# Kernel tuning notes

Hardware: AMD Instinct MI355X
Metric: run time of the kernel (lower is better)

## Reference

```python
import jax, jax.numpy as jnp
import numpy as np

M_MARGIN = 0.25
GAMMA = 64.0
EPS = 1e-5


def _circle_loss_one_way(enc, dec):
    # enc, dec: [N, D]. Faithful to the torch rotate-concat construction:
    # cos_sim[j, k] = cosine(enc[j], dec[(j + k) % N]); column 0 is the positive.
    N = enc.shape[0]
    dot = enc @ dec.T                                   # [N, N]
    en = jnp.sqrt(jnp.sum(enc * enc, axis=1, keepdims=True))   # [N, 1]
    dn = jnp.sqrt(jnp.sum(dec * dec, axis=1, keepdims=True))   # [N, 1]
    S = dot / (en * dn.T + EPS)                         # [N, N] cosine sims
    r = jnp.arange(N)
    idx = (r[:, None] + r[None, :]) % N                 # [N, N] rolled column index
    cos_sim = jnp.take_along_axis(S, idx, axis=1)       # [N, N]
    sp = cos_sim[:, 0:1]                                # [N, 1] positives (diag of S)
    sn = cos_sim[:, 1:]                                 # [N, N-1] negatives
    ap = jnp.maximum(-jax.lax.stop_gradient(sp) + 1.0 + M_MARGIN, 0.0)
    an = jnp.maximum(jax.lax.stop_gradient(sn) + M_MARGIN, 0.0)
    delta_p = 1.0 - M_MARGIN
    delta_n = M_MARGIN
    logit_p = -ap * (sp - delta_p) * GAMMA              # [N, 1]
    logit_n = an * (sn - delta_n) * GAMMA               # [N, N-1]
    lse_n = jax.nn.logsumexp(logit_n, axis=0)           # [N-1]
    lse_p = jax.nn.logsumexp(logit_p, axis=0)           # [1] (cols of repeated sp are identical)
    return jax.nn.softplus(lse_n + lse_p)               # [N-1]


def reference(encoder_output, decoder_output):
    loss_a = _circle_loss_one_way(encoder_output, decoder_output)
    loss_b = _circle_loss_one_way(decoder_output, encoder_output)
    return jnp.mean((loss_a + loss_b) / 2.0)


def setup_inputs() -> dict:
    key = jax.random.key(0)
    k1, k2 = jax.random.split(key)
    N, D = 8192, 128
    return {
        "encoder_output": jax.random.normal(k1, (N, D), dtype=jnp.float32),
        "decoder_output": jax.random.normal(k2, (N, D), dtype=jnp.float32),
    }
```

## Files before the change

kernel.cpp:

```cpp
#include <hip/hip_runtime.h>
#include <hip/hip_bf16.h>

#define NN 8192

using f32x4 = __attribute__((ext_vector_type(4))) float;

#if __has_builtin(__builtin_amdgcn_exp2f)
#define EXP2(x) __builtin_amdgcn_exp2f(x)
#else
#define EXP2(x) __expf((x) * 0.69314718056f)
#endif

__device__ __forceinline__ void gl_lds16(const void* g, void* l) {
  __builtin_amdgcn_global_load_lds(
      (const __attribute__((address_space(1))) unsigned int*)(unsigned long long)g,
      (__attribute__((address_space(3))) unsigned int*)(unsigned int)(unsigned long long)l,
      16, 0, 0);
}

#if __has_builtin(__builtin_amdgcn_cvt_pk_fp8_f32)
__device__ __forceinline__ unsigned pk4_fp8(float x0, float x1, float x2, float x3) {
  unsigned w = (unsigned)__builtin_amdgcn_cvt_pk_fp8_f32(x0, x1, 0, false);
  w = (unsigned)__builtin_amdgcn_cvt_pk_fp8_f32(x2, x3, (int)w, true);
  return w;
}
#else
__device__ __forceinline__ unsigned f8_1(float f) {
  unsigned u = __float_as_uint(f);
  unsigned s = (u >> 24) & 0x80u;
  float a = fabsf(f);
  if (a < 0.015625f) {
    unsigned m = (unsigned)rintf(a * 512.0f);
    return s | (m > 7u ? 8u : m);
  }
  if (a > 448.0f) return s | 0x7Eu;
  unsigned au = u & 0x7FFFFFFFu;
  unsigned e = (au >> 23) - 127u + 7u;
  unsigned m23 = au & 0x7FFFFFu;
  unsigned m = m23 >> 20;
  unsigned rem = m23 & 0xFFFFFu;
  if (rem > 0x80000u || (rem == 0x80000u && (m & 1u))) {
    if (++m == 8u) { m = 0u; ++e; }
  }
  return s | (e << 3) | m;
}
__device__ __forceinline__ unsigned pk4_fp8(float x0, float x1, float x2, float x3) {
  return f8_1(x0) | (f8_1(x1) << 8) | (f8_1(x2) << 16) | (f8_1(x3) << 24);
}
#endif

__global__ __launch_bounds__(256) void k_prep(const float* __restrict__ enc,
                                              const float* __restrict__ dec,
                                              uint2* __restrict__ A8,
                                              uint2* __restrict__ B8,
                                              float* __restrict__ logit_p,
                                              float* __restrict__ bandsum,
                                              unsigned* __restrict__ counter) {
  const int t = threadIdx.x;
  const int l16 = t & 15;
  const int row = blockIdx.x * 16 + (t >> 4);
  const int tid = blockIdx.x * 256 + t;
  if (tid < 64 * 256) bandsum[tid] = 0.0f;
  if (tid == 64 * 256) *counter = 0u;

  const float4* e4 = reinterpret_cast<const float4*>(enc) + (size_t)row * 32 + l16 * 2;
  const float4* d4 = reinterpret_cast<const float4*>(dec) + (size_t)row * 32 + l16 * 2;
  float4 e0 = e4[0], e1 = e4[1];
  float4 d0 = d4[0], d1 = d4[1];

  float se = e0.x*e0.x + e0.y*e0.y + e0.z*e0.z + e0.w*e0.w
           + e1.x*e1.x + e1.y*e1.y + e1.z*e1.z + e1.w*e1.w;
  float sd = d0.x*d0.x + d0.y*d0.y + d0.z*d0.z + d0.w*d0.w
           + d1.x*d1.x + d1.y*d1.y + d1.z*d1.z + d1.w*d1.w;
  float sp = e0.x*d0.x + e0.y*d0.y + e0.z*d0.z + e0.w*d0.w
           + e1.x*d1.x + e1.y*d1.y + e1.z*d1.z + e1.w*d1.w;
#pragma unroll
  for (int off = 1; off < 16; off <<= 1) {
    se += __shfl_xor(se, off);
    sd += __shfl_xor(sd, off);
    sp += __shfl_xor(sp, off);
  }
  float ie = rsqrtf(se), id = rsqrtf(sd);

  uint2 ua, ub;
  ua.x = pk4_fp8(e0.x * ie, e0.y * ie, e0.z * ie, e0.w * ie);
  ua.y = pk4_fp8(e1.x * ie, e1.y * ie, e1.z * ie, e1.w * ie);
  ub.x = pk4_fp8(d0.x * id, d0.y * id, d0.z * id, d0.w * id);
  ub.y = pk4_fp8(d1.x * id, d1.y * id, d1.z * id, d1.w * id);
  A8[(size_t)row * 16 + l16] = ua;
  B8[(size_t)row * 16 + l16] = ub;

  if (l16 == 0) {
    float en = se * ie, dn = sd * id;
    float s  = sp / (en * dn + 1e-5f);
    logit_p[row] = -fmaxf(1.25f - s, 0.0f) * (s - 0.75f) * 64.0f;
  }
}

__global__ __launch_bounds__(256, 2) void k_main(const unsigned char* __restrict__ A,
                                                 const unsigned char* __restrict__ B,
                                                 float* __restrict__ bandsum,
                                                 const float* __restrict__ logit_p,
                                                 unsigned* __restrict__ counter,
                                                 float* __restrict__ out) {
  __shared__ __align__(16) unsigned char As[2 * 16384];
  __shared__ __align__(16) unsigned char Bs[2 * 16384];
  __shared__ float part[4][256];
  __shared__ unsigned lastFlag;

  const int t  = threadIdx.x;
  const int T  = blockIdx.x;
  const int sp = blockIdx.y;

#pragma unroll
  for (int q = 0; q < 4; ++q) part[q][t] = 0.0f;

  const int lane = t & 63;
  const int w = t >> 6, wrow = w >> 1, wcol = w & 1;
  const int l15 = lane & 15, quad = lane >> 4;
  const int x7 = l15 & 7;
  const int qh = quad >> 1, ql8 = (quad & 1) * 8;

  const int rl = t >> 3;
  const int lgoff = rl * 128 + ((t & 7) ^ (rl & 7)) * 16;
  const int lloff = t * 16;

  const char* Ab = (const char*)A;
  const char* Bb = (const char*)B;

  float dreg[28];
#pragma unroll
  for (int i = 0; i < 28; ++i) dreg[i] = 0.0f;

  const int arow = (wrow * 64 + l15) * 128;
  const int brow = (wcol * 64 + l15) * 128;

  {
    const int by = sp * 8;
    const int bx = (by + T) & 63;
    const char* Ag = Ab + (size_t)by * 16384 + lgoff;
    const char* Bg = Bb + (size_t)bx * 16384 + lgoff;
#pragma unroll
    for (int j = 0; j < 4; ++j) {
      gl_lds16(Ag + j * 4096, (char*)As + j * 4096 + lloff);
      gl_lds16(Bg + j * 4096, (char*)Bs + j * 4096 + lloff);
    }
  }
  __syncthreads();

  for (int it = 0; it < 8; ++it) {
    const int p = it & 1;

    if (it < 7) {
      const int by = sp * 8 + it + 1;
      const int bx = (by + T) & 63;
      const char* Ag = Ab + (size_t)by * 16384 + lgoff;
      const char* Bg = Bb + (size_t)bx * 16384 + lgoff;
      char* Ad = (char*)As + (p ^ 1) * 16384 + lloff;
      char* Bd = (char*)Bs + (p ^ 1) * 16384 + lloff;
#pragma unroll
      for (int j = 0; j < 4; ++j) {
        gl_lds16(Ag + j * 4096, Ad + j * 4096);
        gl_lds16(Bg + j * 4096, Bd + j * 4096);
      }
    }

    f32x4 acc[4][4];
    const f32x4 zv = {0.f, 0.f, 0.f, 0.f};
#pragma unroll
    for (int r = 0; r < 4; ++r)
#pragma unroll
      for (int c = 0; c < 4; ++c) acc[r][c] = zv;

    const char* Abuf = (const char*)As + p * 16384;
    const char* Bbuf = (const char*)Bs + p * 16384;

#pragma unroll
    for (int ks = 0; ks < 4; ++ks) {
      long a[4], b[4];
      const int off = (((ks * 2 + qh) ^ x7) * 16) + ql8;
#pragma unroll
      for (int r = 0; r < 4; ++r)
        a[r] = *reinterpret_cast<const long*>(Abuf + arow + r * 2048 + off);
#pragma unroll
      for (int c = 0; c < 4; ++c)
        b[c] = *reinterpret_cast<const long*>(Bbuf + brow + c * 2048 + off);
#pragma unroll
      for (int r = 0; r < 4; ++r)
#pragma unroll
        for (int c = 0; c < 4; ++c)
          acc[r][c] = __builtin_amdgcn_mfma_f32_16x16x32_fp8_fp8(a[r], b[c], acc[r][c], 0, 0, 0);
    }

#pragma unroll
    for (int dlt = -3; dlt <= 3; ++dlt) {
#pragma unroll
      for (int g = 0; g < 4; ++g) {
        float s = 0.0f;
#pragma unroll
        for (int r = 0; r < 4; ++r) {
          int c = r + dlt;
          if (c < 0 || c > 3) continue;
          float sn = acc[r][c][g];
          float an = fmaxf(sn + 0.25f, 0.0f);
          float u  = fmaf(sn, 92.332483f, -23.083121f);
          s += EXP2(an * u);
        }
        dreg[(dlt + 3) * 4 + g] += s;
      }
    }

    __syncthreads();
  }

  const int  Qoff = (wcol - wrow) * 64 + 127;
  const int  v    = l15 - quad * 4;
  const bool leader = (quad == 0) || (l15 <= 3);
  const bool ok1 = (l15 <= 11) && (quad <= 2);
  const bool ok2 = (l15 <= 7)  && (quad <= 1);

#pragma unroll
  for (int dlt = -3; dlt <= 3; ++dlt) {
#pragma unroll
    for (int g = 0; g < 4; ++g) {
      float s = dreg[(dlt + 3) * 4 + g];
      float t1 = __shfl_down(s, 20); s += ok1 ? t1 : 0.0f;
      float t2 = __shfl_down(s, 40); s += ok2 ? t2 : 0.0f;
      int ld = Qoff + dlt * 16 - g + v;
      if (leader) unsafeAtomicAdd(&part[w][ld], s);
    }
  }
  __syncthreads();

  if (t < 255) {
    float vv = part[0][t] + part[1][t] + part[2][t] + part[3][t];
    unsafeAtomicAdd(&bandsum[T * 256 + t], vv);
  }

  __syncthreads();
  if (t == 0) lastFlag = (atomicAdd(counter, 1u) == 511u) ? 1u : 0u;
  __syncthreads();
  if (!lastFlag) return;

  __threadfence();
  float* sm = part[0];

  float lp[32];
#pragma unroll
  for (int k = 0; k < 32; ++k) lp[k] = logit_p[t + 256 * k];

  float m = lp[0];
#pragma unroll
  for (int k = 1; k < 32; ++k) m = fmaxf(m, lp[k]);
#pragma unroll
  for (int off = 32; off; off >>= 1) m = fmaxf(m, __shfl_down(m, off));
  if (lane == 0) sm[w] = m;
  __syncthreads();
  m = fmaxf(fmaxf(sm[0], sm[1]), fmaxf(sm[2], sm[3]));
  __syncthreads();

  float s = 0.0f;
#pragma unroll
  for (int k = 0; k < 32; ++k) s += __expf(lp[k] - m);
#pragma unroll
  for (int off = 32; off; off >>= 1) s += __shfl_down(s, off);
  if (lane == 0) sm[w] = s;
  __syncthreads();
  s = sm[0] + sm[1] + sm[2] + sm[3];
  float lse_p = m + __logf(s);
  __syncthreads();

  const int o  = t & 127;
  const int hi = t >> 7;
  float bs1[32], bs2[32];
#pragma unroll
  for (int k = 0; k < 32; ++k) {
    int Ta = hi + 2 * k;
    bs1[k] = bandsum[Ta * 256 + o + 127];
    bs2[k] = o ? bandsum[((Ta + 1) & 63) * 256 + o - 1] : 0.0f;
  }
  float acc = 0.0f;
#pragma unroll
  for (int k = 0; k < 32; ++k) {
    if (t == 0 && k == 0) continue;
    float se = bs1[k] + bs2[k];
    float x = __logf(se) + lse_p;
    acc += fmaxf(x, 0.0f) + __logf(1.0f + __expf(-fabsf(x)));
  }
#pragma unroll
  for (int off = 32; off; off >>= 1) acc += __shfl_down(acc, off);
  if (lane == 0) sm[w] = acc;
  __syncthreads();
  if (t == 0) out[0] = (sm[0] + sm[1] + sm[2] + sm[3]) * (1.0f / 8191.0f);
}

extern "C" void kernel_launch(void* const* d_in, const int* in_sizes, int n_in,
                              void* d_out, int out_size, void* d_ws, size_t ws_size,
                              hipStream_t stream) {
  const float* enc = (const float*)d_in[0];
  const float* dec = (const float*)d_in[1];
  float* ws = (float*)d_ws;

  float*    logit_p = ws;
  float*    bandsum = ws + 8192;
  unsigned* counter = (unsigned*)(ws + 8192 + 16384);
  uint2*    A8      = (uint2*)(ws + 8192 + 16384 + 256);
  uint2*    B8      = (uint2*)((char*)A8 + 1048576);
  float*    out     = (float*)d_out;

  k_prep<<<NN / 16, 256, 0, stream>>>(enc, dec, A8, B8, logit_p, bandsum, counter);
  dim3 grid(64, 8);
  k_main<<<grid, 256, 0, stream>>>((const unsigned char*)A8, (const unsigned char*)B8,
                                   bandsum, logit_p, counter, out);
}
```

Baseline: 96.51 us.

## Split K into halves to shrink LDS tiles and double grid/occupancy

Each 128x128 fp8 tile is now loaded as two 64-byte K halves, which halves the LDS staging buffers. The accumulator persists across the pair, and the epilogue runs only after the second half. The grid doubles to 64x16 blocks with four tiles each, and launch bounds move to 4 blocks per SM so more waves can hide latency. The trade-off is twice as many synchronizations per tile and tighter register limits that may cause spills.

```diff
diff --git a/kernel.cpp b/kernel.cpp
--- a/kernel.cpp
+++ b/kernel.cpp
@@ -97,14 +97,14 @@
   }
 }
 
-__global__ __launch_bounds__(256, 2) void k_main(const unsigned char* __restrict__ A,
+__global__ __launch_bounds__(256, 4) void k_main(const unsigned char* __restrict__ A,
                                                  const unsigned char* __restrict__ B,
                                                  float* __restrict__ bandsum,
                                                  const float* __restrict__ logit_p,
                                                  unsigned* __restrict__ counter,
                                                  float* __restrict__ out) {
-  __shared__ __align__(16) unsigned char As[2 * 16384];
-  __shared__ __align__(16) unsigned char Bs[2 * 16384];
+  __shared__ __align__(16) unsigned char As[2 * 8192];
+  __shared__ __align__(16) unsigned char Bs[2 * 8192];
   __shared__ float part[4][256];
   __shared__ unsigned lastFlag;
 
@@ -118,11 +118,10 @@
   const int lane = t & 63;
   const int w = t >> 6, wrow = w >> 1, wcol = w & 1;
   const int l15 = lane & 15, quad = lane >> 4;
-  const int x7 = l15 & 7;
+  const int x3 = l15 & 3;
   const int qh = quad >> 1, ql8 = (quad & 1) * 8;
 
-  const int rl = t >> 3;
-  const int lgoff = rl * 128 + ((t & 7) ^ (rl & 7)) * 16;
+  const int lg    = (t >> 2) * 128 + (((t & 3) ^ ((t >> 2) & 3)) * 16);
   const int lloff = t * 16;
 
   const char* Ab = (const char*)A;
@@ -132,59 +131,64 @@
 #pragma unroll
   for (int i = 0; i < 28; ++i) dreg[i] = 0.0f;
 
-  const int arow = (wrow * 64 + l15) * 128;
-  const int brow = (wcol * 64 + l15) * 128;
+  const int arow = (wrow * 64 + l15) * 64;
+  const int brow = (wcol * 64 + l15) * 64;
 
   {
-    const int by = sp * 8;
+    const int by = sp * 4;
     const int bx = (by + T) & 63;
-    const char* Ag = Ab + (size_t)by * 16384 + lgoff;
-    const char* Bg = Bb + (size_t)bx * 16384 + lgoff;
-#pragma unroll
-    for (int j = 0; j < 4; ++j) {
-      gl_lds16(Ag + j * 4096, (char*)As + j * 4096 + lloff);
-      gl_lds16(Bg + j * 4096, (char*)Bs + j * 4096 + lloff);
-    }
-  }
-  __syncthreads();
-
-  for (int it = 0; it < 8; ++it) {
-    const int p = it & 1;
-
-    if (it < 7) {
-      const int by = sp * 8 + it + 1;
+    const char* Ag = Ab + (size_t)by * 16384 + lg;
+    const char* Bg = Bb + (size_t)bx * 16384 + lg;
+#pragma unroll
+    for (int j = 0; j < 2; ++j) {
+      gl_lds16(Ag + j * 8192, (char*)As + j * 4096 + lloff);
+      gl_lds16(Bg + j * 8192, (char*)Bs + j * 4096 + lloff);
+    }
+  }
+  __syncthreads();
+
+  f32x4 acc[4][4];
+
+#pragma unroll
+  for (int h = 0; h < 8; ++h) {
+    const int p = h & 1;
+
+    if (h < 7) {
+      const int hn = h + 1;
+      const int by = sp * 4 + (hn >> 1);
       const int bx = (by + T) & 63;
-      const char* Ag = Ab + (size_t)by * 16384 + lgoff;
-      const char* Bg = Bb + (size_t)bx * 16384 + lgoff;
-      char* Ad = (char*)As + (p ^ 1) * 16384 + lloff;
-      char* Bd = (char*)Bs + (p ^ 1) * 16384 + lloff;
-#pragma unroll
-      for (int j = 0; j < 4; ++j) {
-        gl_lds16(Ag + j * 4096, Ad + j * 4096);
-        gl_lds16(Bg + j * 4096, Bd + j * 4096);
+      const char* Ag = Ab + (size_t)by * 16384 + (hn & 1) * 64 + lg;
+      const char* Bg = Bb + (size_t)bx * 16384 + (hn & 1) * 64 + lg;
+      char* Ad = (char*)As + (p ^ 1) * 8192 + lloff;
+      char* Bd = (char*)Bs + (p ^ 1) * 8192 + lloff;
+#pragma unroll
+      for (int j = 0; j < 2; ++j) {
+        gl_lds16(Ag + j * 8192, Ad + j * 4096);
+        gl_lds16(Bg + j * 8192, Bd + j * 4096);
       }
     }
 
-    f32x4 acc[4][4];
-    const f32x4 zv = {0.f, 0.f, 0.f, 0.f};
-#pragma unroll
-    for (int r = 0; r < 4; ++r)
-#pragma unroll
-      for (int c = 0; c < 4; ++c) acc[r][c] = zv;
-
-    const char* Abuf = (const char*)As + p * 16384;
-    const char* Bbuf = (const char*)Bs + p * 16384;
-
-#pragma unroll
-    for (int ks = 0; ks < 4; ++ks) {
+    if (p == 0) {
+      const f32x4 zv = {0.f, 0.f, 0.f, 0.f};
+#pragma unroll
+      for (int r = 0; r < 4; ++r)
+#pragma unroll
+        for (int c = 0; c < 4; ++c) acc[r][c] = zv;
+    }
+
+    const char* Abuf = (const char*)As + p * 8192;
+    const char* Bbuf = (const char*)Bs + p * 8192;
+
+#pragma unroll
+    for (int ks = 0; ks < 2; ++ks) {
       long a[4], b[4];
-      const int off = (((ks * 2 + qh) ^ x7) * 16) + ql8;
+      const int off = (((ks * 2 + qh) ^ x3) * 16) + ql8;
 #pragma unroll
       for (int r = 0; r < 4; ++r)
-        a[r] = *reinterpret_cast<const long*>(Abuf + arow + r * 2048 + off);
+        a[r] = *reinterpret_cast<const long*>(Abuf + arow + r * 1024 + off);
 #pragma unroll
       for (int c = 0; c < 4; ++c)
-        b[c] = *reinterpret_cast<const long*>(Bbuf + brow + c * 2048 + off);
+        b[c] = *reinterpret_cast<const long*>(Bbuf + brow + c * 1024 + off);
 #pragma unroll
       for (int r = 0; r < 4; ++r)
 #pragma unroll
@@ -192,21 +196,23 @@
           acc[r][c] = __builtin_amdgcn_mfma_f32_16x16x32_fp8_fp8(a[r], b[c], acc[r][c], 0, 0, 0);
     }
 
-#pragma unroll
-    for (int dlt = -3; dlt <= 3; ++dlt) {
-#pragma unroll
-      for (int g = 0; g < 4; ++g) {
-        float s = 0.0f;
-#pragma unroll
-        for (int r = 0; r < 4; ++r) {
-          int c = r + dlt;
-          if (c < 0 || c > 3) continue;
-          float sn = acc[r][c][g];
-          float an = fmaxf(sn + 0.25f, 0.0f);
-          float u  = fmaf(sn, 92.332483f, -23.083121f);
-          s += EXP2(an * u);
+    if (p == 1) {
+#pragma unroll
+      for (int dlt = -3; dlt <= 3; ++dlt) {
+#pragma unroll
+        for (int g = 0; g < 4; ++g) {
+          float s = 0.0f;
+#pragma unroll
+          for (int r = 0; r < 4; ++r) {
+            int c = r + dlt;
+            if (c < 0 || c > 3) continue;
+            float sn = acc[r][c][g];
+            float an = fmaxf(sn + 0.25f, 0.0f);
+            float u  = fmaf(sn, 92.332483f, -23.083121f);
+            s += EXP2(an * u);
+          }
+          dreg[(dlt + 3) * 4 + g] += s;
         }
-        dreg[(dlt + 3) * 4 + g] += s;
       }
     }
 
@@ -238,7 +244,7 @@
   }
 
   __syncthreads();
-  if (t == 0) lastFlag = (atomicAdd(counter, 1u) == 511u) ? 1u : 0u;
+  if (t == 0) lastFlag = (atomicAdd(counter, 1u) == 1023u) ? 1u : 0u;
   __syncthreads();
   if (!lastFlag) return;
 
@@ -279,17 +285,17 @@
     bs1[k] = bandsum[Ta * 256 + o + 127];
     bs2[k] = o ? bandsum[((Ta + 1) & 63) * 256 + o - 1] : 0.0f;
   }
-  float acc = 0.0f;
+  float tacc = 0.0f;
 #pragma unroll
   for (int k = 0; k < 32; ++k) {
     if (t == 0 && k == 0) continue;
     float se = bs1[k] + bs2[k];
     float x = __logf(se) + lse_p;
-    acc += fmaxf(x, 0.0f) + __logf(1.0f + __expf(-fabsf(x)));
-  }
-#pragma unroll
-  for (int off = 32; off; off >>= 1) acc += __shfl_down(acc, off);
-  if (lane == 0) sm[w] = acc;
+    tacc += fmaxf(x, 0.0f) + __logf(1.0f + __expf(-fabsf(x)));
+  }
+#pragma unroll
+  for (int off = 32; off; off >>= 1) tacc += __shfl_down(tacc, off);
+  if (lane == 0) sm[w] = tacc;
   __syncthreads();
   if (t == 0) out[0] = (sm[0] + sm[1] + sm[2] + sm[3]) * (1.0f / 8191.0f);
 }
@@ -309,7 +315,7 @@
   float*    out     = (float*)d_out;
 
   k_prep<<<NN / 16, 256, 0, stream>>>(enc, dec, A8, B8, logit_p, bandsum, counter);
-  dim3 grid(64, 8);
+  dim3 grid(64, 16);
   k_main<<<grid, 256, 0, stream>>>((const unsigned char*)A8, (const unsigned char*)B8,
                                    bandsum, logit_p, counter, out);
 }
```

New measurement: 210.4 us. 2.18x slower.

## Software-pipeline MFMA and exp epilogue across two accumulator sets

Applied to the files above, without the earlier changes.

Restructures the main loop so the MFMA tile products for one iteration are issued while the exp-based epilogue of the previous iteration runs. Two accumulator arrays alternate, so the matrix-core work and the VALU/transcendental work can interleave within a wave. This doubles accumulator register use (32 more f32x4), which risks spills or lower occupancy under launch_bounds(256,2).

```diff
diff --git a/kernel.cpp b/kernel.cpp
--- a/kernel.cpp
+++ b/kernel.cpp
@@ -97,6 +97,53 @@
   }
 }
 
+__device__ __forceinline__ void mfma_win(f32x4 (&acc)[4][4],
+                                         const unsigned char* __restrict__ Abuf,
+                                         const unsigned char* __restrict__ Bbuf,
+                                         int arow, int brow, int qh, int x7, int ql8) {
+  const f32x4 zv = {0.f, 0.f, 0.f, 0.f};
+#pragma unroll
+  for (int r = 0; r < 4; ++r)
+#pragma unroll
+    for (int c = 0; c < 4; ++c) acc[r][c] = zv;
+#pragma unroll
+  for (int ks = 0; ks < 4; ++ks) {
+    long a[4], b[4];
+    const int off = (((ks * 2 + qh) ^ x7) * 16) + ql8;
+#pragma unroll
+    for (int r = 0; r < 4; ++r)
+      a[r] = *reinterpret_cast<const long*>(Abuf + arow + r * 2048 + off);
+#pragma unroll
+    for (int c = 0; c < 4; ++c)
+      b[c] = *reinterpret_cast<const long*>(Bbuf + brow + c * 2048 + off);
+#pragma unroll
+    for (int r = 0; r < 4; ++r)
+#pragma unroll
+      for (int c = 0; c < 4; ++c)
+        acc[r][c] = __builtin_amdgcn_mfma_f32_16x16x32_fp8_fp8(a[r], b[c], acc[r][c], 0, 0, 0);
+  }
+}
+
+__device__ __forceinline__ void epi_win(const f32x4 (&acc)[4][4], float (&dreg)[28]) {
+#pragma unroll
+  for (int dlt = -3; dlt <= 3; ++dlt) {
+#pragma unroll
+    for (int g = 0; g < 4; ++g) {
+      float s = 0.0f;
+#pragma unroll
+      for (int r = 0; r < 4; ++r) {
+        int c = r + dlt;
+        if (c < 0 || c > 3) continue;
+        float sn = acc[r][c][g];
+        float an = fmaxf(sn + 0.25f, 0.0f);
+        float u  = fmaf(sn, 92.332483f, -23.083121f);
+        s += EXP2(an * u);
+      }
+      dreg[(dlt + 3) * 4 + g] += s;
+    }
+  }
+}
+
 __global__ __launch_bounds__(256, 2) void k_main(const unsigned char* __restrict__ A,
                                                  const unsigned char* __restrict__ B,
                                                  float* __restrict__ bandsum,
@@ -135,83 +182,50 @@
   const int arow = (wrow * 64 + l15) * 128;
   const int brow = (wcol * 64 + l15) * 128;
 
-  {
-    const int by = sp * 8;
+  auto stage = [&](int itn) {
+    const int by = sp * 8 + itn;
     const int bx = (by + T) & 63;
     const char* Ag = Ab + (size_t)by * 16384 + lgoff;
     const char* Bg = Bb + (size_t)bx * 16384 + lgoff;
+    char* Ad = (char*)As + (itn & 1) * 16384 + lloff;
+    char* Bd = (char*)Bs + (itn & 1) * 16384 + lloff;
 #pragma unroll
     for (int j = 0; j < 4; ++j) {
-      gl_lds16(Ag + j * 4096, (char*)As + j * 4096 + lloff);
-      gl_lds16(Bg + j * 4096, (char*)Bs + j * 4096 + lloff);
+      gl_lds16(Ag + j * 4096, Ad + j * 4096);
+      gl_lds16(Bg + j * 4096, Bd + j * 4096);
     }
-  }
-  __syncthreads();
-
-  for (int it = 0; it < 8; ++it) {
-    const int p = it & 1;
-
-    if (it < 7) {
-      const int by = sp * 8 + it + 1;
-      const int bx = (by + T) & 63;
-      const char* Ag = Ab + (size_t)by * 16384 + lgoff;
-      const char* Bg = Bb + (size_t)bx * 16384 + lgoff;
-      char* Ad = (char*)As + (p ^ 1) * 16384 + lloff;
-      char* Bd = (char*)Bs + (p ^ 1) * 16384 + lloff;
-#pragma unroll
-      for (int j = 0; j < 4; ++j) {
-        gl_lds16(Ag + j * 4096, Ad + j * 4096);
-        gl_lds16(Bg + j * 4096, Bd + j * 4096);
-      }
-    }
-
-    f32x4 acc[4][4];
-    const f32x4 zv = {0.f, 0.f, 0.f, 0.f};
-#pragma unroll
-    for (int r = 0; r < 4; ++r)
-#pragma unroll
-      for (int c = 0; c < 4; ++c) acc[r][c] = zv;
-
-    const char* Abuf = (const char*)As + p * 16384;
-    const char* Bbuf = (const char*)Bs + p * 16384;
-
-#pragma unroll
-    for (int ks = 0; ks < 4; ++ks) {
-      long a[4], b[4];
-      const int off = (((ks * 2 + qh) ^ x7) * 16) + ql8;
-#pragma unroll
-      for (int r = 0; r < 4; ++r)
-        a[r] = *reinterpret_cast<const long*>(Abuf + arow + r * 2048 + off);
-#pragma unroll
-      for (int c = 0; c < 4; ++c)
-        b[c] = *reinterpret_cast<const long*>(Bbuf + brow + c * 2048 + off);
-#pragma unroll
-      for (int r = 0; r < 4; ++r)
-#pragma unroll
-        for (int c = 0; c < 4; ++c)
-          acc[r][c] = __builtin_amdgcn_mfma_f32_16x16x32_fp8_fp8(a[r], b[c], acc[r][c], 0, 0, 0);
-    }
-
-#pragma unroll
-    for (int dlt = -3; dlt <= 3; ++dlt) {
-#pragma unroll
-      for (int g = 0; g < 4; ++g) {
-        float s = 0.0f;
-#pragma unroll
-        for (int r = 0; r < 4; ++r) {
-          int c = r + dlt;
-          if (c < 0 || c > 3) continue;
-          float sn = acc[r][c][g];
-          float an = fmaxf(sn + 0.25f, 0.0f);
-          float u  = fmaf(sn, 92.332483f, -23.083121f);
-          s += EXP2(an * u);
-        }
-        dreg[(dlt + 3) * 4 + g] += s;
-      }
-    }
-
+  };
+
+  const unsigned char* As0 = (const unsigned char*)As;
+  const unsigned char* Bs0 = (const unsigned char*)Bs;
+  const unsigned char* As1 = (const unsigned char*)As + 16384;
+  const unsigned char* Bs1 = (const unsigned char*)Bs + 16384;
+
+  f32x4 accA[4][4], accB[4][4];
+
+  stage(0);
+  __syncthreads();
+
+  stage(1);
+  mfma_win(accA, As0, Bs0, arow, brow, qh, x7, ql8);
+  __syncthreads();
+
+  for (int it = 1; it < 7; it += 2) {
+    stage(it + 1);
+    mfma_win(accB, As1, Bs1, arow, brow, qh, x7, ql8);
+    epi_win(accA, dreg);
     __syncthreads();
-  }
+
+    stage(it + 2);
+    mfma_win(accA, As0, Bs0, arow, brow, qh, x7, ql8);
+    epi_win(accB, dreg);
+    __syncthreads();
+  }
+
+  mfma_win(accB, As1, Bs1, arow, brow, qh, x7, ql8);
+  epi_win(accA, dreg);
+  epi_win(accB, dreg);
+  __syncthreads();
 
   const int  Qoff = (wcol - wrow) * 64 + 127;
   const int  v    = l15 - quad * 4;
@@ -279,17 +293,17 @@
     bs1[k] = bandsum[Ta * 256 + o + 127];
     bs2[k] = o ? bandsum[((Ta + 1) & 63) * 256 + o - 1] : 0.0f;
   }
-  float acc = 0.0f;
+  float tacc = 0.0f;
 #pragma unroll
   for (int k = 0; k < 32; ++k) {
     if (t == 0 && k == 0) continue;
     float se = bs1[k] + bs2[k];
     float x = __logf(se) + lse_p;
-    acc += fmaxf(x, 0.0f) + __logf(1.0f + __expf(-fabsf(x)));
-  }
-#pragma unroll
-  for (int off = 32; off; off >>= 1) acc += __shfl_down(acc, off);
-  if (lane == 0) sm[w] = acc;
+    tacc += fmaxf(x, 0.0f) + __logf(1.0f + __expf(-fabsf(x)));
+  }
+#pragma unroll
+  for (int off = 32; off; off >>= 1) tacc += __shfl_down(tacc, off);
+  if (lane == 0) sm[w] = tacc;
   __syncthreads();
   if (t == 0) out[0] = (sm[0] + sm[1] + sm[2] + sm[3]) * (1.0f / 8191.0f);
 }
```

Result: slower. 109.1 us (+13.0%).
